# Kernel tuning notes

Measured on AMD Instinct MI355X. Metric: run time of the kernel, lower is better.

Reference implementation:

```python
import jax, jax.numpy as jnp
import numpy as np

# init config (matches init_kwargs)
NO_TRANS = False
SPATIAL_SCALE = 0.0625
POOLED = 7
SAMPLES = 2          # sampling_ratio (sample_per_part)
TRANS_STD = 0.1

B, C, H, W = 2, 256, 96, 96
N_ROIS = 512


def setup_inputs() -> dict:
    key = jax.random.key(0)
    k1, k2, k3, k4, k5 = jax.random.split(key, 5)
    bottom_data = jax.random.normal(k1, (B, C, H, W), dtype=jnp.float32)
    img = H / SPATIAL_SCALE  # image-space extent (1536)
    bidx = jax.random.randint(k2, (N_ROIS,), 0, B).astype(jnp.float32)
    xy1 = jax.random.uniform(k3, (N_ROIS, 2), minval=0.0, maxval=0.7 * img)
    wh = jax.random.uniform(k4, (N_ROIS, 2), minval=0.05 * img, maxval=0.3 * img)
    bottom_rois = jnp.concatenate([bidx[:, None], xy1, xy1 + wh], axis=1)  # [N,5]
    bottom_trans = jax.random.normal(k5, (N_ROIS, 2, POOLED, POOLED), dtype=jnp.float32)
    return {"bottom_data": bottom_data, "bottom_rois": bottom_rois, "bottom_trans": bottom_trans}


def _deform_psroi_pool(feat, rois, trans):
    # feat [B,C,H,W], rois [N,5], trans [N,2,P,P] -> out [N,C,P,P]
    Hf, Wf = feat.shape[2], feat.shape[3]
    b = rois[:, 0].astype(jnp.int32)                                    # [N]
    # CUDA kernel rounds roi coords, shifts by -0.5
    x1 = jnp.round(rois[:, 1]) * SPATIAL_SCALE - 0.5
    y1 = jnp.round(rois[:, 2]) * SPATIAL_SCALE - 0.5
    x2 = (jnp.round(rois[:, 3]) + 1.0) * SPATIAL_SCALE - 0.5
    y2 = (jnp.round(rois[:, 4]) + 1.0) * SPATIAL_SCALE - 0.5
    rw = jnp.maximum(x2 - x1, 0.1)
    rh = jnp.maximum(y2 - y1, 0.1)
    bin_w = rw / POOLED
    bin_h = rh / POOLED
    sub_w = bin_w / SAMPLES
    sub_h = bin_h / SAMPLES

    grid = jnp.arange(POOLED, dtype=feat.dtype)
    # part_size == pooled_size and group_size == 1 -> part_h=ph, part_w=pw, class 0
    if NO_TRANS:
        trans_x = jnp.zeros((rois.shape[0], POOLED, POOLED), feat.dtype)
        trans_y = trans_x
    else:
        trans_x = trans[:, 0] * TRANS_STD  # [N,P,P]
        trans_y = trans[:, 1] * TRANS_STD

    # bin start coords per (n, ph, pw)
    wstart = grid[None, None, :] * bin_w[:, None, None] + x1[:, None, None] + trans_x * rw[:, None, None]
    hstart = grid[None, :, None] * bin_h[:, None, None] + y1[:, None, None] + trans_y * rh[:, None, None]

    s = jnp.arange(SAMPLES, dtype=feat.dtype)
    # sample coords [N,P,P,S(ih),S(iw)]
    w = wstart[:, :, :, None, None] + s[None, None, None, None, :] * sub_w[:, None, None, None, None]
    h = hstart[:, :, :, None, None] + s[None, None, None, :, None] * sub_h[:, None, None, None, None]

    valid = (w >= -0.5) & (w <= Wf - 0.5) & (h >= -0.5) & (h <= Hf - 0.5)
    wc = jnp.clip(w, 0.0, Wf - 1.0)
    hc = jnp.clip(h, 0.0, Hf - 1.0)
    x0 = jnp.floor(wc); y0 = jnp.floor(hc)
    dx = wc - x0; dy = hc - y0
    x0i = x0.astype(jnp.int32); y0i = y0.astype(jnp.int32)
    x1i = jnp.ceil(wc).astype(jnp.int32); y1i = jnp.ceil(hc).astype(jnp.int32)

    feat_hwc = jnp.transpose(feat, (0, 2, 3, 1))  # [B,H,W,C]
    bb = b[:, None, None, None, None]

    def gather(yi, xi):
        return feat_hwc[bb, yi, xi]  # [N,P,P,S,S,C]

    w00 = ((1.0 - dx) * (1.0 - dy))[..., None]
    w01 = (dx * (1.0 - dy))[..., None]
    w10 = ((1.0 - dx) * dy)[..., None]
    w11 = (dx * dy)[..., None]
    val = (w00 * gather(y0i, x0i) + w01 * gather(y0i, x1i)
           + w10 * gather(y1i, x0i) + w11 * gather(y1i, x1i))
    val = jnp.where(valid[..., None], val, 0.0)

    ssum = val.sum(axis=(3, 4))                              # [N,P,P,C]
    count = valid.astype(feat.dtype).sum(axis=(3, 4))        # [N,P,P]
    out = jnp.where(count[..., None] > 0, ssum / jnp.maximum(count[..., None], 1.0), 0.0)
    return jnp.transpose(out, (0, 3, 1, 2))                  # [N,C,P,P]


def reference(bottom_data, bottom_rois, bottom_trans):
    return _deform_psroi_pool(bottom_data, bottom_rois, bottom_trans)
```

## Files before the change

### kernel.cpp

```cpp
#include <hip/hip_runtime.h>

#define B_      2
#define C_      256
#define H_      96
#define W_      96
#define HW_     (H_ * W_)
#define P_      7
#define PP_     (P_ * P_)
#define NROIS_  512
#define SCALE_  0.0625f
#define TSTD_   0.1f

#define NGROUP_ 8
#define GC_     (C_ / NGROUP_)

typedef float vf4 __attribute__((ext_vector_type(4)));

__device__ __forceinline__ unsigned f2bf(float f) {
    union { float f; unsigned u; } x; x.f = f;
    return (x.u + 0x7fffu + ((x.u >> 16) & 1u)) >> 16;
}
__device__ __forceinline__ float bf_lo(unsigned u) {
    union { unsigned i; float f; } x; x.i = u << 16; return x.f;
}
__device__ __forceinline__ float bf_hi(unsigned u) {
    union { unsigned i; float f; } x; x.i = u & 0xffff0000u; return x.f;
}

__global__ __launch_bounds__(256) void nchw_to_gp_bf16(const float* __restrict__ in,
                                                       ushort* __restrict__ out) {
    __shared__ float tile[32][36];
    const int b   = blockIdx.z;
    const int g   = blockIdx.x & (NGROUP_ - 1);
    const int p0  = (blockIdx.x >> 3) * 32;
    const int c0  = g * 32;
    const int tid = threadIdx.x;

    const float* src = in + (size_t)b * (C_ * HW_);
    ushort*      dst = out + ((size_t)(b * NGROUP_ + g) * HW_) * GC_;

    {
        const int cr = tid >> 3;
        const int pq = (tid & 7) * 4;
        const vf4 v = __builtin_nontemporal_load(
            (const vf4*)&src[(size_t)(c0 + cr) * HW_ + p0 + pq]);
        *(vf4*)&tile[cr][pq] = v;
    }
    __syncthreads();

    {
        const int p  = tid >> 3;
        const int cq = (tid & 7) * 4;
        uint2 o;
        o.x = f2bf(tile[cq + 0][p]) | (f2bf(tile[cq + 1][p]) << 16);
        o.y = f2bf(tile[cq + 2][p]) | (f2bf(tile[cq + 3][p]) << 16);
        *(uint2*)&((unsigned*)dst)[(size_t)(p0 + p) * (GC_ / 2) + (cq >> 1)] = o;
    }
}

__global__ __launch_bounds__(256, 4) void dpsroi_pool7(const ushort* __restrict__ feat,
                                                       const float* __restrict__ rois,
                                                       const float* __restrict__ trans,
                                                       float* __restrict__ out) {
    __shared__ float sout[GC_ * PP_];

    const int blk = blockIdx.x;
    const int g   = blk & (NGROUP_ - 1);
    const int n   = blk >> 3;
    const int tid = threadIdx.x;
    const int bin = tid >> 2;
    const int ch0 = (tid & 3) * 8;

    const int   broi = (int)rois[n * 5 + 0];
    const float x1 = rintf(rois[n * 5 + 1]) * SCALE_ - 0.5f;
    const float y1 = rintf(rois[n * 5 + 2]) * SCALE_ - 0.5f;
    const float x2 = (rintf(rois[n * 5 + 3]) + 1.0f) * SCALE_ - 0.5f;
    const float y2 = (rintf(rois[n * 5 + 4]) + 1.0f) * SCALE_ - 0.5f;
    const float rw = fmaxf(x2 - x1, 0.1f);
    const float rh = fmaxf(y2 - y1, 0.1f);
    const float bin_w = rw * (1.0f / 7.0f);
    const float bin_h = rh * (1.0f / 7.0f);
    const float sub_w = bin_w * 0.5f;
    const float sub_h = bin_h * 0.5f;

    const ushort* fb = feat + ((size_t)(broi * NGROUP_ + g) * HW_) * GC_ + ch0;

    if (bin < PP_) {
        const int pi = bin / P_;
        const int pj = bin - pi * P_;
        const float tx = trans[((n * 2 + 0) * P_ + pi) * P_ + pj] * TSTD_;
        const float ty = trans[((n * 2 + 1) * P_ + pi) * P_ + pj] * TSTD_;
        const float wstart = (float)pj * bin_w + x1 + tx * rw;
        const float hstart = (float)pi * bin_h + y1 + ty * rh;

        float wt[16];
        int   ofs[16];
        int   cnt = 0;
#pragma unroll
        for (int s = 0; s < 4; ++s) {
            const float w = wstart + (float)(s & 1) * sub_w;
            const float h = hstart + (float)(s >> 1) * sub_h;
            const bool valid = (w >= -0.5f) & (w <= (float)W_ - 0.5f) &
                               (h >= -0.5f) & (h <= (float)H_ - 0.5f);
            cnt += valid ? 1 : 0;
            const float vf = valid ? 1.0f : 0.0f;
            const float wc  = fminf(fmaxf(w, 0.0f), (float)(W_ - 1));
            const float hc  = fminf(fmaxf(h, 0.0f), (float)(H_ - 1));
            const float x0f = floorf(wc), y0f = floorf(hc);
            const float dx  = wc - x0f,   dy  = hc - y0f;
            const int   x0  = (int)x0f,   y0  = (int)y0f;
            const int   xp  = (int)ceilf(wc), yp = (int)ceilf(hc);
            wt[4 * s + 0] = vf * (1.0f - dx) * (1.0f - dy);
            wt[4 * s + 1] = vf * dx * (1.0f - dy);
            wt[4 * s + 2] = vf * (1.0f - dx) * dy;
            wt[4 * s + 3] = vf * dx * dy;
            ofs[4 * s + 0] = y0 * W_ + x0;
            ofs[4 * s + 1] = y0 * W_ + xp;
            ofs[4 * s + 2] = yp * W_ + x0;
            ofs[4 * s + 3] = yp * W_ + xp;
        }

        uint4 v[16];
#pragma unroll
        for (int i = 0; i < 16; ++i)
            v[i] = *(const uint4*)(fb + (size_t)ofs[i] * GC_);

        float acc[8] = {0.f, 0.f, 0.f, 0.f, 0.f, 0.f, 0.f, 0.f};
#pragma unroll
        for (int i = 0; i < 16; ++i) {
            const float wgt = wt[i];
            acc[0] += wgt * bf_lo(v[i].x);
            acc[1] += wgt * bf_hi(v[i].x);
            acc[2] += wgt * bf_lo(v[i].y);
            acc[3] += wgt * bf_hi(v[i].y);
            acc[4] += wgt * bf_lo(v[i].z);
            acc[5] += wgt * bf_hi(v[i].z);
            acc[6] += wgt * bf_lo(v[i].w);
            acc[7] += wgt * bf_hi(v[i].w);
        }

        const float inv = (cnt > 0) ? (1.0f / (float)cnt) : 0.0f;
#pragma unroll
        for (int j = 0; j < 8; ++j)
            sout[(ch0 + j) * PP_ + bin] = acc[j] * inv;
    }

    __syncthreads();
    float* outn = out + ((size_t)n * C_ + g * GC_) * PP_;
    for (int f = tid; f < GC_ * PP_; f += 256)
        __builtin_nontemporal_store(sout[f], &outn[f]);
}

extern "C" void kernel_launch(void* const* d_in, const int* in_sizes, int n_in,
                              void* d_out, int out_size, void* d_ws, size_t ws_size,
                              hipStream_t stream) {
    const float* feat  = (const float*)d_in[0];
    const float* rois  = (const float*)d_in[1];
    const float* trans = (const float*)d_in[2];
    float* out = (float*)d_out;

    ushort* gp = (ushort*)d_ws;
    dim3 tb(256);
    dim3 tg((HW_ / 32) * NGROUP_, 1, B_);
    nchw_to_gp_bf16<<<tg, tb, 0, stream>>>(feat, gp);
    dpsroi_pool7<<<NROIS_ * NGROUP_, 256, 0, stream>>>(gp, rois, trans, out);
}
```

Before: 91.11 us.

## Split bilinear x-neighbours across thread pairs with packed FMA and LDS trans table

The pooling kernel now uses 8 threads per bin instead of 4, at 448 threads per block. The two halves of each thread group take the left and right bilinear column. Because the channel-group layout stores pixel x0+1 right after x0, the right column is reached by reading the adjacent 32 channels, and a zero pad is written past the workspace end for the last pixel. Per-thread loads drop from 16 to 8, accumulation uses packed vf2 FMAs, and partial sums are combined with a shuffle. Trans values for the ROI are staged in shared memory. The aim is more parallelism and memory-level concurrency per bin, at the cost of shuffles, a larger block and reliance on zero-weight reads across row boundaries.

```diff
diff --git a/kernel.cpp b/kernel.cpp
--- a/kernel.cpp
+++ b/kernel.cpp
@@ -14,17 +14,19 @@
 #define NGROUP_ 8
 #define GC_     (C_ / NGROUP_)
 
+#define TPB2_   448
+
 typedef float vf4 __attribute__((ext_vector_type(4)));
+typedef float vf2 __attribute__((ext_vector_type(2)));
 
 __device__ __forceinline__ unsigned f2bf(float f) {
     union { float f; unsigned u; } x; x.f = f;
     return (x.u + 0x7fffu + ((x.u >> 16) & 1u)) >> 16;
 }
-__device__ __forceinline__ float bf_lo(unsigned u) {
-    union { unsigned i; float f; } x; x.i = u << 16; return x.f;
-}
-__device__ __forceinline__ float bf_hi(unsigned u) {
-    union { unsigned i; float f; } x; x.i = u & 0xffff0000u; return x.f;
+__device__ __forceinline__ vf2 bfpair(unsigned u) {
+    union { unsigned i; float f; } lo, hi;
+    lo.i = u << 16; hi.i = u & 0xffff0000u;
+    vf2 r; r.x = lo.f; r.y = hi.f; return r;
 }
 
 __global__ __launch_bounds__(256) void nchw_to_gp_bf16(const float* __restrict__ in,
@@ -35,6 +37,9 @@
     const int p0  = (blockIdx.x >> 3) * 32;
     const int c0  = g * 32;
     const int tid = threadIdx.x;
+
+    if (blockIdx.x == 0 && blockIdx.z == 0 && tid < 32)
+        out[(size_t)B_ * NGROUP_ * HW_ * GC_ + tid] = (ushort)0;
 
     const float* src = in + (size_t)b * (C_ * HW_);
     ushort*      dst = out + ((size_t)(b * NGROUP_ + g) * HW_) * GC_;
@@ -58,18 +63,23 @@
     }
 }
 
-__global__ __launch_bounds__(256, 4) void dpsroi_pool7(const ushort* __restrict__ feat,
-                                                       const float* __restrict__ rois,
-                                                       const float* __restrict__ trans,
-                                                       float* __restrict__ out) {
+__global__ __launch_bounds__(TPB2_, 6) void dpsroi_pool7(const ushort* __restrict__ feat,
+                                                         const float* __restrict__ rois,
+                                                         const float* __restrict__ trans,
+                                                         float* __restrict__ out) {
     __shared__ float sout[GC_ * PP_];
+    __shared__ float ttab[2 * PP_];
 
     const int blk = blockIdx.x;
     const int g   = blk & (NGROUP_ - 1);
     const int n   = blk >> 3;
     const int tid = threadIdx.x;
-    const int bin = tid >> 2;
-    const int ch0 = (tid & 3) * 8;
+    const int bin = tid >> 3;
+    const int q   = tid & 7;
+    const int px  = q >> 2;
+    const int ch0 = (q & 3) * 8;
+
+    if (tid < 2 * PP_) ttab[tid] = trans[n * (2 * PP_) + tid];
 
     const int   broi = (int)rois[n * 5 + 0];
     const float x1 = rintf(rois[n * 5 + 1]) * SCALE_ - 0.5f;
@@ -83,18 +93,20 @@
     const float sub_w = bin_w * 0.5f;
     const float sub_h = bin_h * 0.5f;
 
-    const ushort* fb = feat + ((size_t)(broi * NGROUP_ + g) * HW_) * GC_ + ch0;
+    __syncthreads();
+
+    const ushort* fb = feat + ((size_t)(broi * NGROUP_ + g) * HW_) * GC_ + q * 8;
 
     if (bin < PP_) {
         const int pi = bin / P_;
         const int pj = bin - pi * P_;
-        const float tx = trans[((n * 2 + 0) * P_ + pi) * P_ + pj] * TSTD_;
-        const float ty = trans[((n * 2 + 1) * P_ + pi) * P_ + pj] * TSTD_;
+        const float tx = ttab[bin] * TSTD_;
+        const float ty = ttab[PP_ + bin] * TSTD_;
         const float wstart = (float)pj * bin_w + x1 + tx * rw;
         const float hstart = (float)pi * bin_h + y1 + ty * rh;
 
-        float wt[16];
-        int   ofs[16];
+        float wt[8];
+        int   ofs[8];
         int   cnt = 0;
 #pragma unroll
         for (int s = 0; s < 4; ++s) {
@@ -109,45 +121,42 @@
             const float x0f = floorf(wc), y0f = floorf(hc);
             const float dx  = wc - x0f,   dy  = hc - y0f;
             const int   x0  = (int)x0f,   y0  = (int)y0f;
-            const int   xp  = (int)ceilf(wc), yp = (int)ceilf(hc);
-            wt[4 * s + 0] = vf * (1.0f - dx) * (1.0f - dy);
-            wt[4 * s + 1] = vf * dx * (1.0f - dy);
-            wt[4 * s + 2] = vf * (1.0f - dx) * dy;
-            wt[4 * s + 3] = vf * dx * dy;
-            ofs[4 * s + 0] = y0 * W_ + x0;
-            ofs[4 * s + 1] = y0 * W_ + xp;
-            ofs[4 * s + 2] = yp * W_ + x0;
-            ofs[4 * s + 3] = yp * W_ + xp;
+            const int   yp  = (int)ceilf(hc);
+            const float wx  = vf * (px ? dx : (1.0f - dx));
+            wt[2 * s + 0] = wx * (1.0f - dy);
+            wt[2 * s + 1] = wx * dy;
+            ofs[2 * s + 0] = y0 * W_ + x0;
+            ofs[2 * s + 1] = yp * W_ + x0;
         }
 
-        uint4 v[16];
+        uint4 v[8];
 #pragma unroll
-        for (int i = 0; i < 16; ++i)
+        for (int i = 0; i < 8; ++i)
             v[i] = *(const uint4*)(fb + (size_t)ofs[i] * GC_);
 
-        float acc[8] = {0.f, 0.f, 0.f, 0.f, 0.f, 0.f, 0.f, 0.f};
+        vf2 a01 = {0.f, 0.f}, a23 = {0.f, 0.f}, a45 = {0.f, 0.f}, a67 = {0.f, 0.f};
 #pragma unroll
-        for (int i = 0; i < 16; ++i) {
-            const float wgt = wt[i];
-            acc[0] += wgt * bf_lo(v[i].x);
-            acc[1] += wgt * bf_hi(v[i].x);
-            acc[2] += wgt * bf_lo(v[i].y);
-            acc[3] += wgt * bf_hi(v[i].y);
-            acc[4] += wgt * bf_lo(v[i].z);
-            acc[5] += wgt * bf_hi(v[i].z);
-            acc[6] += wgt * bf_lo(v[i].w);
-            acc[7] += wgt * bf_hi(v[i].w);
+        for (int i = 0; i < 8; ++i) {
+            vf2 w2; w2.x = wt[i]; w2.y = wt[i];
+            a01 = __builtin_elementwise_fma(w2, bfpair(v[i].x), a01);
+            a23 = __builtin_elementwise_fma(w2, bfpair(v[i].y), a23);
+            a45 = __builtin_elementwise_fma(w2, bfpair(v[i].z), a45);
+            a67 = __builtin_elementwise_fma(w2, bfpair(v[i].w), a67);
         }
 
+        float a[8] = { a01.x, a01.y, a23.x, a23.y, a45.x, a45.y, a67.x, a67.y };
         const float inv = (cnt > 0) ? (1.0f / (float)cnt) : 0.0f;
 #pragma unroll
-        for (int j = 0; j < 8; ++j)
-            sout[(ch0 + j) * PP_ + bin] = acc[j] * inv;
+        for (int j = 0; j < 8; ++j) {
+            const float s2 = a[j] + __shfl_xor(a[j], 4);
+            if (px == 0)
+                sout[(ch0 + j) * PP_ + bin] = s2 * inv;
+        }
     }
 
     __syncthreads();
     float* outn = out + ((size_t)n * C_ + g * GC_) * PP_;
-    for (int f = tid; f < GC_ * PP_; f += 256)
+    for (int f = tid; f < GC_ * PP_; f += TPB2_)
         __builtin_nontemporal_store(sout[f], &outn[f]);
 }
 
@@ -163,5 +172,5 @@
     dim3 tb(256);
     dim3 tg((HW_ / 32) * NGROUP_, 1, B_);
     nchw_to_gp_bf16<<<tg, tb, 0, stream>>>(feat, gp);
-    dpsroi_pool7<<<NROIS_ * NGROUP_, 256, 0, stream>>>(gp, rois, trans, out);
+    dpsroi_pool7<<<NROIS_ * NGROUP_, TPB2_, 0, stream>>>(gp, rois, trans, out);
 }
```

Measured after the change: 95.09 us. +4.4%, slower.

## Stage ROI feature patch in shared memory before bilinear sampling

Applied to the files above, without the earlier changes.

Each block now computes the bounding box of all sample points of its ROI, cooperatively copies that patch of the bf16 feature map (for its channel group) into LDS, and serves the 16 bilinear taps from LDS instead of scattered global loads. Larger ROIs fall back to the old global-gather path. Trans values are also staged in LDS. It adds extra syncs, atomics and about 72KB of LDS per block, and lowers launch_bounds occupancy to 2. The goal is coalesced loads instead of redundant scattered ones, at the cost of occupancy and of loading patch pixels that no sample uses.

```diff
diff --git a/kernel.cpp b/kernel.cpp
--- a/kernel.cpp
+++ b/kernel.cpp
@@ -14,6 +14,9 @@
 #define NGROUP_ 8
 #define GC_     (C_ / NGROUP_)
 
+#define PATCH_MAX 1120
+#define PSPIX_    (PATCH_MAX + 2)
+
 typedef float vf4 __attribute__((ext_vector_type(4)));
 
 __device__ __forceinline__ unsigned f2bf(float f) {
@@ -47,7 +50,6 @@
         *(vf4*)&tile[cr][pq] = v;
     }
     __syncthreads();
-
     {
         const int p  = tid >> 3;
         const int cq = (tid & 7) * 4;
@@ -58,18 +60,25 @@
     }
 }
 
-__global__ __launch_bounds__(256, 4) void dpsroi_pool7(const ushort* __restrict__ feat,
+__global__ __launch_bounds__(256, 2) void dpsroi_pool7(const ushort* __restrict__ feat,
                                                        const float* __restrict__ rois,
                                                        const float* __restrict__ trans,
                                                        float* __restrict__ out) {
+    __shared__ uint4 patch[4 * PSPIX_];
     __shared__ float sout[GC_ * PP_];
+    __shared__ float ttab[2 * PP_];
+    __shared__ int   bb[4];
 
     const int blk = blockIdx.x;
     const int g   = blk & (NGROUP_ - 1);
     const int n   = blk >> 3;
     const int tid = threadIdx.x;
     const int bin = tid >> 2;
-    const int ch0 = (tid & 3) * 8;
+    const int chq = tid & 3;
+    const int ch0 = chq * 8;
+
+    if (tid < 2 * PP_) ttab[tid] = trans[n * (2 * PP_) + tid];
+    if (tid == 0) { bb[0] = 1 << 30; bb[1] = -(1 << 30); bb[2] = 1 << 30; bb[3] = -(1 << 30); }
 
     const int   broi = (int)rois[n * 5 + 0];
     const float x1 = rintf(rois[n * 5 + 1]) * SCALE_ - 0.5f;
@@ -83,19 +92,52 @@
     const float sub_w = bin_w * 0.5f;
     const float sub_h = bin_h * 0.5f;
 
-    const ushort* fb = feat + ((size_t)(broi * NGROUP_ + g) * HW_) * GC_ + ch0;
-
+    __syncthreads();
+
+    float wstart = 0.f, hstart = 0.f;
     if (bin < PP_) {
         const int pi = bin / P_;
         const int pj = bin - pi * P_;
-        const float tx = trans[((n * 2 + 0) * P_ + pi) * P_ + pj] * TSTD_;
-        const float ty = trans[((n * 2 + 1) * P_ + pi) * P_ + pj] * TSTD_;
-        const float wstart = (float)pj * bin_w + x1 + tx * rw;
-        const float hstart = (float)pi * bin_h + y1 + ty * rh;
-
+        const float tx = ttab[bin] * TSTD_;
+        const float ty = ttab[PP_ + bin] * TSTD_;
+        wstart = (float)pj * bin_w + x1 + tx * rw;
+        hstart = (float)pi * bin_h + y1 + ty * rh;
+        if (chq == 0) {
+            const int xlo = (int)floorf(fminf(fmaxf(wstart, 0.0f), (float)(W_ - 1)));
+            const int xhi = (int)ceilf (fminf(fmaxf(wstart + sub_w, 0.0f), (float)(W_ - 1)));
+            const int ylo = (int)floorf(fminf(fmaxf(hstart, 0.0f), (float)(H_ - 1)));
+            const int yhi = (int)ceilf (fminf(fmaxf(hstart + sub_h, 0.0f), (float)(H_ - 1)));
+            atomicMin(&bb[0], xlo); atomicMax(&bb[1], xhi);
+            atomicMin(&bb[2], ylo); atomicMax(&bb[3], yhi);
+        }
+    }
+    __syncthreads();
+
+    const int bx0 = bb[0], bx1 = bb[1], by0 = bb[2], by1 = bb[3];
+    const int pw = bx1 - bx0 + 1;
+    const int ph = by1 - by0 + 1;
+    const bool use_patch = (pw * ph <= PATCH_MAX);
+
+    const ushort* fb0 = feat + ((size_t)(broi * NGROUP_ + g) * HW_) * GC_;
+
+    if (use_patch) {
+        const uint4* src = (const uint4*)fb0;
+        const int pw4   = pw * 4;
+        const int total = ph * pw4;
+        for (int q = tid; q < total; q += 256) {
+            const int py  = q / pw4;
+            const int r   = q - py * pw4;
+            const int pxl = r >> 2;
+            const int cq  = r & 3;
+            patch[cq * PSPIX_ + py * pw + pxl] = src[((by0 + py) * W_ + bx0) * 4 + r];
+        }
+        __syncthreads();
+    }
+
+    if (bin < PP_) {
         float wt[16];
-        int   ofs[16];
-        int   cnt = 0;
+        int xs0[4], xs1[4], ys0[4], ys1[4];
+        int cnt = 0;
 #pragma unroll
         for (int s = 0; s < 4; ++s) {
             const float w = wstart + (float)(s & 1) * sub_w;
@@ -108,22 +150,36 @@
             const float hc  = fminf(fmaxf(h, 0.0f), (float)(H_ - 1));
             const float x0f = floorf(wc), y0f = floorf(hc);
             const float dx  = wc - x0f,   dy  = hc - y0f;
-            const int   x0  = (int)x0f,   y0  = (int)y0f;
-            const int   xp  = (int)ceilf(wc), yp = (int)ceilf(hc);
+            xs0[s] = (int)x0f;            ys0[s] = (int)y0f;
+            xs1[s] = (int)ceilf(wc);      ys1[s] = (int)ceilf(hc);
             wt[4 * s + 0] = vf * (1.0f - dx) * (1.0f - dy);
             wt[4 * s + 1] = vf * dx * (1.0f - dy);
             wt[4 * s + 2] = vf * (1.0f - dx) * dy;
             wt[4 * s + 3] = vf * dx * dy;
-            ofs[4 * s + 0] = y0 * W_ + x0;
-            ofs[4 * s + 1] = y0 * W_ + xp;
-            ofs[4 * s + 2] = yp * W_ + x0;
-            ofs[4 * s + 3] = yp * W_ + xp;
         }
 
         uint4 v[16];
-#pragma unroll
-        for (int i = 0; i < 16; ++i)
-            v[i] = *(const uint4*)(fb + (size_t)ofs[i] * GC_);
+        if (use_patch) {
+            const uint4* pp = patch + chq * PSPIX_;
+#pragma unroll
+            for (int s = 0; s < 4; ++s) {
+                const int r0 = (ys0[s] - by0) * pw - bx0;
+                const int r1 = (ys1[s] - by0) * pw - bx0;
+                v[4 * s + 0] = pp[r0 + xs0[s]];
+                v[4 * s + 1] = pp[r0 + xs1[s]];
+                v[4 * s + 2] = pp[r1 + xs0[s]];
+                v[4 * s + 3] = pp[r1 + xs1[s]];
+            }
+        } else {
+            const ushort* fbq = fb0 + ch0;
+#pragma unroll
+            for (int s = 0; s < 4; ++s) {
+                v[4 * s + 0] = *(const uint4*)(fbq + (size_t)(ys0[s] * W_ + xs0[s]) * GC_);
+                v[4 * s + 1] = *(const uint4*)(fbq + (size_t)(ys0[s] * W_ + xs1[s]) * GC_);
+                v[4 * s + 2] = *(const uint4*)(fbq + (size_t)(ys1[s] * W_ + xs0[s]) * GC_);
+                v[4 * s + 3] = *(const uint4*)(fbq + (size_t)(ys1[s] * W_ + xs1[s]) * GC_);
+            }
+        }
 
         float acc[8] = {0.f, 0.f, 0.f, 0.f, 0.f, 0.f, 0.f, 0.f};
 #pragma unroll
```

Result: slower. 134.2 us (+47.3%).

## Stage trans offsets in shared memory and interleave loads with accumulation

Applied to the files above, without the earlier changes.

Raises the launch-bounds occupancy hint for the pooling kernel from 4 to 8 blocks per CU. It also restructures the inner loop so each sample's four bilinear loads are consumed right away instead of holding 16 uint4 loads in registers at once. The per-ROI trans values are loaded once into shared memory, which adds a block-wide barrier. The aim is lower register pressure and more waves in flight to hide gather latency. The cost is less memory-level parallelism per thread, though the compiler may still hoist the loads after unrolling.

```diff
diff --git a/kernel.cpp b/kernel.cpp
--- a/kernel.cpp
+++ b/kernel.cpp
@@ -47,7 +47,6 @@
         *(vf4*)&tile[cr][pq] = v;
     }
     __syncthreads();
-
     {
         const int p  = tid >> 3;
         const int cq = (tid & 7) * 4;
@@ -58,11 +57,12 @@
     }
 }
 
-__global__ __launch_bounds__(256, 4) void dpsroi_pool7(const ushort* __restrict__ feat,
+__global__ __launch_bounds__(256, 8) void dpsroi_pool7(const ushort* __restrict__ feat,
                                                        const float* __restrict__ rois,
                                                        const float* __restrict__ trans,
                                                        float* __restrict__ out) {
     __shared__ float sout[GC_ * PP_];
+    __shared__ float ttab[2 * PP_];
 
     const int blk = blockIdx.x;
     const int g   = blk & (NGROUP_ - 1);
@@ -70,6 +70,8 @@
     const int tid = threadIdx.x;
     const int bin = tid >> 2;
     const int ch0 = (tid & 3) * 8;
+
+    if (tid < 2 * PP_) ttab[tid] = trans[n * (2 * PP_) + tid];
 
     const int   broi = (int)rois[n * 5 + 0];
     const float x1 = rintf(rois[n * 5 + 1]) * SCALE_ - 0.5f;
@@ -83,19 +85,21 @@
     const float sub_w = bin_w * 0.5f;
     const float sub_h = bin_h * 0.5f;
 
+    __syncthreads();
+
     const ushort* fb = feat + ((size_t)(broi * NGROUP_ + g) * HW_) * GC_ + ch0;
 
     if (bin < PP_) {
         const int pi = bin / P_;
         const int pj = bin - pi * P_;
-        const float tx = trans[((n * 2 + 0) * P_ + pi) * P_ + pj] * TSTD_;
-        const float ty = trans[((n * 2 + 1) * P_ + pi) * P_ + pj] * TSTD_;
+        const float tx = ttab[bin] * TSTD_;
+        const float ty = ttab[PP_ + bin] * TSTD_;
         const float wstart = (float)pj * bin_w + x1 + tx * rw;
         const float hstart = (float)pi * bin_h + y1 + ty * rh;
 
-        float wt[16];
-        int   ofs[16];
+        float acc[8] = {0.f, 0.f, 0.f, 0.f, 0.f, 0.f, 0.f, 0.f};
         int   cnt = 0;
+
 #pragma unroll
         for (int s = 0; s < 4; ++s) {
             const float w = wstart + (float)(s & 1) * sub_w;
@@ -110,33 +114,36 @@
             const float dx  = wc - x0f,   dy  = hc - y0f;
             const int   x0  = (int)x0f,   y0  = (int)y0f;
             const int   xp  = (int)ceilf(wc), yp = (int)ceilf(hc);
-            wt[4 * s + 0] = vf * (1.0f - dx) * (1.0f - dy);
-            wt[4 * s + 1] = vf * dx * (1.0f - dy);
-            wt[4 * s + 2] = vf * (1.0f - dx) * dy;
-            wt[4 * s + 3] = vf * dx * dy;
-            ofs[4 * s + 0] = y0 * W_ + x0;
-            ofs[4 * s + 1] = y0 * W_ + xp;
-            ofs[4 * s + 2] = yp * W_ + x0;
-            ofs[4 * s + 3] = yp * W_ + xp;
-        }
 
-        uint4 v[16];
-#pragma unroll
-        for (int i = 0; i < 16; ++i)
-            v[i] = *(const uint4*)(fb + (size_t)ofs[i] * GC_);
+            const uint4 v0 = *(const uint4*)(fb + (size_t)(y0 * W_ + x0) * GC_);
+            const uint4 v1 = *(const uint4*)(fb + (size_t)(y0 * W_ + xp) * GC_);
+            const uint4 v2 = *(const uint4*)(fb + (size_t)(yp * W_ + x0) * GC_);
+            const uint4 v3 = *(const uint4*)(fb + (size_t)(yp * W_ + xp) * GC_);
 
-        float acc[8] = {0.f, 0.f, 0.f, 0.f, 0.f, 0.f, 0.f, 0.f};
-#pragma unroll
-        for (int i = 0; i < 16; ++i) {
-            const float wgt = wt[i];
-            acc[0] += wgt * bf_lo(v[i].x);
-            acc[1] += wgt * bf_hi(v[i].x);
-            acc[2] += wgt * bf_lo(v[i].y);
-            acc[3] += wgt * bf_hi(v[i].y);
-            acc[4] += wgt * bf_lo(v[i].z);
-            acc[5] += wgt * bf_hi(v[i].z);
-            acc[6] += wgt * bf_lo(v[i].w);
-            acc[7] += wgt * bf_hi(v[i].w);
+            const float w00 = vf * (1.0f - dx) * (1.0f - dy);
+            const float w01 = vf * dx * (1.0f - dy);
+            const float w10 = vf * (1.0f - dx) * dy;
+            const float w11 = vf * dx * dy;
+
+            acc[0] += w00 * bf_lo(v0.x); acc[1] += w00 * bf_hi(v0.x);
+            acc[2] += w00 * bf_lo(v0.y); acc[3] += w00 * bf_hi(v0.y);
+            acc[4] += w00 * bf_lo(v0.z); acc[5] += w00 * bf_hi(v0.z);
+            acc[6] += w00 * bf_lo(v0.w); acc[7] += w00 * bf_hi(v0.w);
+
+            acc[0] += w01 * bf_lo(v1.x); acc[1] += w01 * bf_hi(v1.x);
+            acc[2] += w01 * bf_lo(v1.y); acc[3] += w01 * bf_hi(v1.y);
+            acc[4] += w01 * bf_lo(v1.z); acc[5] += w01 * bf_hi(v1.z);
+            acc[6] += w01 * bf_lo(v1.w); acc[7] += w01 * bf_hi(v1.w);
+
+            acc[0] += w10 * bf_lo(v2.x); acc[1] += w10 * bf_hi(v2.x);
+            acc[2] += w10 * bf_lo(v2.y); acc[3] += w10 * bf_hi(v2.y);
+            acc[4] += w10 * bf_lo(v2.z); acc[5] += w10 * bf_hi(v2.z);
+            acc[6] += w10 * bf_lo(v2.w); acc[7] += w10 * bf_hi(v2.w);
+
+            acc[0] += w11 * bf_lo(v3.x); acc[1] += w11 * bf_hi(v3.x);
+            acc[2] += w11 * bf_lo(v3.y); acc[3] += w11 * bf_hi(v3.y);
+            acc[4] += w11 * bf_lo(v3.z); acc[5] += w11 * bf_hi(v3.z);
+            acc[6] += w11 * bf_lo(v3.w); acc[7] += w11 * bf_hi(v3.w);
         }
 
         const float inv = (cnt > 0) ? (1.0f / (float)cnt) : 0.0f;
```

Result: slower. 128.4 us (+40.9%).
